# Kernel tuning notes

Hardware: AMD Instinct MI355X
Metric: run time of the kernel (lower is better)

The kernel has to match this reference:

```python
import jax, jax.numpy as jnp
import numpy as np

B = 65536
IN_DIM = 1280
E = 8          # num_experts
H1 = 256       # hidden_dim
H2 = 128       # hidden_dim // 2


def setup_inputs() -> dict:
    key = jax.random.key(0)
    ks = jax.random.split(key, 9)
    s1 = 1.0 / np.sqrt(IN_DIM)
    s2 = 1.0 / np.sqrt(H1)
    s3 = 1.0 / np.sqrt(H2)
    return {
        "x":  jax.random.normal(ks[0], (B, IN_DIM), dtype=jnp.float32),
        # stacked expert params: layer1 [E,in,H1], layer2 [E,H1,H2], layer3 [E,H2]
        "W1": jax.random.uniform(ks[1], (E, IN_DIM, H1), jnp.float32, -s1, s1),
        "b1": jax.random.uniform(ks[2], (E, H1), jnp.float32, -s1, s1),
        "W2": jax.random.uniform(ks[3], (E, H1, H2), jnp.float32, -s2, s2),
        "b2": jax.random.uniform(ks[4], (E, H2), jnp.float32, -s2, s2),
        "W3": jax.random.uniform(ks[5], (E, H2), jnp.float32, -s3, s3),
        "b3": jax.random.uniform(ks[6], (E,), jnp.float32, -s3, s3),
        # gate params [in,E]
        "Wg": jax.random.uniform(ks[7], (IN_DIM, E), jnp.float32, -s1, s1),
        "bg": jax.random.uniform(ks[8], (E,), jnp.float32, -s1, s1),
    }


def reference(x, W1, b1, W2, b2, W3, b3, Wg, bg):
    # All E experts run densely on every token (dropout = eval/identity).
    h1 = jax.nn.relu(jnp.einsum("bi,eih->beh", x, W1) + b1)          # [B,E,H1]
    h2 = jax.nn.relu(jnp.einsum("beh,ehk->bek", h1, W2) + b2)        # [B,E,H2]
    expert_out = jnp.einsum("bek,ek->be", h2, W3) + b3               # [B,E]
    gate = jax.nn.softmax(x @ Wg + bg, axis=-1)                      # [B,E]
    predictions = jnp.sum(expert_out * gate, axis=1)                 # [B]
    return predictions, gate
```

## Files before the change

kernel.cpp:

```cpp
#include <hip/hip_runtime.h>
#include <stdint.h>

#define NTOK 65536
#define KDIM 1280

typedef __attribute__((ext_vector_type(8))) short short8;
typedef __attribute__((ext_vector_type(4))) float floatx4;

__device__ __forceinline__ unsigned short f2bf(float f) {
  union { float f; unsigned int u; } v; v.f = f;
  unsigned int r = v.u + 0x7FFFu + ((v.u >> 16) & 1u);
  return (unsigned short)(r >> 16);
}

__device__ __forceinline__ unsigned cvtpk(float lo, float hi) {
  unsigned r;
  asm("v_cvt_pk_bf16_f32 %0, %1, %2" : "=v"(r) : "v"(lo), "v"(hi));
  return r;
}

#define GLDS16(gp, lp) \
  __builtin_amdgcn_global_load_lds((const __attribute__((address_space(1))) void*)(gp), \
                                   (__attribute__((address_space(3))) void*)(lp), 16, 0, 0)


__global__ __launch_bounds__(256)
void pack_all_kernel(const float* __restrict__ W1, const float* __restrict__ W2,
                     const float* __restrict__ Wg,
                     unsigned short* __restrict__ W1t, unsigned short* __restrict__ W2t,
                     unsigned short* __restrict__ WgTb) {
  int t = blockIdx.x * 256 + threadIdx.x;
  if (t < 327680) {
    int n = t / 160, kg = t - n * 160;
    int e = n >> 8, h = n & 255;
    int k = kg * 8;
    const float* src = W1 + ((size_t)e * 1280 + k) * 256 + h;
    uint4 o;
    o.x = (unsigned)f2bf(src[0])       | ((unsigned)f2bf(src[256])     << 16);
    o.y = (unsigned)f2bf(src[2 * 256]) | ((unsigned)f2bf(src[3 * 256]) << 16);
    o.z = (unsigned)f2bf(src[4 * 256]) | ((unsigned)f2bf(src[5 * 256]) << 16);
    o.w = (unsigned)f2bf(src[6 * 256]) | ((unsigned)f2bf(src[7 * 256]) << 16);
    *(uint4*)(W1t + (size_t)n * 1280 + k) = o;
  } else if (t < 360448) {
    int t2 = t - 327680;
    int ng = t2 >> 5, kg = t2 & 31;
    int e = ng >> 7, n = ng & 127;
    int k = kg * 8;
    const float* src = W2 + (size_t)e * 32768 + (size_t)k * 128 + n;
    uint4 o;
    o.x = (unsigned)f2bf(src[0])       | ((unsigned)f2bf(src[128])     << 16);
    o.y = (unsigned)f2bf(src[2 * 128]) | ((unsigned)f2bf(src[3 * 128]) << 16);
    o.z = (unsigned)f2bf(src[4 * 128]) | ((unsigned)f2bf(src[5 * 128]) << 16);
    o.w = (unsigned)f2bf(src[6 * 128]) | ((unsigned)f2bf(src[7 * 128]) << 16);
    *(uint4*)(W2t + (size_t)ng * 256 + k) = o;
  } else {
    int t3 = t - 360448;
    int e = t3 / 1280, k = t3 - e * 1280;
    WgTb[t3] = (e < 8) ? f2bf(Wg[(size_t)k * 8 + e]) : (unsigned short)0;
  }
}


__global__ __launch_bounds__(256, 3)
void expert_fused_kernel(const float* __restrict__ xf,
                         const unsigned short* __restrict__ W1t,
                         const float* __restrict__ b1,
                         const unsigned short* __restrict__ W2t,
                         const float* __restrict__ b2,
                         const float* __restrict__ W3,
                         const float* __restrict__ b3,
                         const unsigned short* __restrict__ WgTb,
                         const float* __restrict__ bg,
                         float* __restrict__ outG,
                         float* __restrict__ eo) {
  __shared__ __align__(16) unsigned short smem[24576];
  unsigned short* WsA = smem;
  unsigned short* WsB = smem + 8192;
  unsigned short* XsA = smem + 16384;
  unsigned short* XsB = smem + 18432;
  unsigned short* h1L = smem;
  unsigned short* W2A = smem + 16384;
  unsigned short* W2B = smem + 20480;
  unsigned short* WgA = smem + 20480;
  unsigned short* WgB = smem + 21504;

  const int tid = threadIdx.x;
  const int wv = tid >> 6;
  const int lane = tid & 63;

  const int wg = blockIdx.x + (blockIdx.y << 3);
  const int c  = wg & 7;
  const int w  = wg >> 3;
  const int e  = w & 7;
  const int m0 = ((c << 7) + (w >> 3)) << 6;
  const bool gate_blk = (e == 0);

  const unsigned short* W1te = W1t + (size_t)e * 256 * 1280;
  const unsigned short* W2te = W2t + (size_t)e * 128 * 256;

  const int lr = lane >> 2;
  const int ksw = ((lane & 3) ^ ((lane >> 3) & 3)) * 8;
  const int fr = lane & 15;
  const int fkS = (((lane >> 4) ^ ((lane >> 1) & 3)) & 3) * 8;
  const int fkL = (lane >> 4) * 8;
  const int rq = (lane >> 4) * 4;

  const float* gxf = xf + (size_t)(m0 + wv * 16 + lr) * 1280 + ksw;
  const unsigned short* gw = W1te + (size_t)(wv * 64 + lr) * 1280 + ksw;
  const unsigned short* gwg = WgTb + (size_t)lr * 1280 + ksw;
  unsigned short* lwA = &WsA[(wv * 64) * 32];
  unsigned short* lwB = &WsB[(wv * 64) * 32];
  const bool gate_stager = gate_blk && (wv == 0);

  floatx4 acc1[4][4] = {};
  floatx4 accg = {0.f, 0.f, 0.f, 0.f};
  for (int k0 = 0; k0 < 1280; k0 += 64) {
    float4 xa0 = *(const float4*)(gxf + k0);
    float4 xa1 = *(const float4*)(gxf + k0 + 4);
    float4 xb0 = *(const float4*)(gxf + k0 + 32);
    float4 xb1 = *(const float4*)(gxf + k0 + 36);
#pragma unroll
    for (int r = 0; r < 4; r++) {
      GLDS16(gw + (size_t)(16 * r) * 1280 + k0, lwA + r * 16 * 32);
      GLDS16(gw + (size_t)(16 * r) * 1280 + k0 + 32, lwB + r * 16 * 32);
    }
    if (gate_stager) { GLDS16(gwg + k0, WgA); GLDS16(gwg + k0 + 32, WgB); }
    uint4 pa, pb;
    pa.x = cvtpk(xa0.x, xa0.y); pa.y = cvtpk(xa0.z, xa0.w);
    pa.z = cvtpk(xa1.x, xa1.y); pa.w = cvtpk(xa1.z, xa1.w);
    pb.x = cvtpk(xb0.x, xb0.y); pb.y = cvtpk(xb0.z, xb0.w);
    pb.z = cvtpk(xb1.x, xb1.y); pb.w = cvtpk(xb1.z, xb1.w);
    *(uint4*)&XsA[(wv * 16 + lr) * 32 + (lane & 3) * 8] = pa;
    *(uint4*)&XsB[(wv * 16 + lr) * 32 + (lane & 3) * 8] = pb;
    __syncthreads();
    {
      short8 bfv[4];
#pragma unroll
      for (int j = 0; j < 4; j++)
        bfv[j] = *(const short8*)&XsA[(j * 16 + fr) * 32 + fkS];
#pragma unroll
      for (int i = 0; i < 4; i++) {
        short8 af = *(const short8*)&WsA[(wv * 64 + i * 16 + fr) * 32 + fkS];
#pragma unroll
        for (int j = 0; j < 4; j++)
          acc1[i][j] = __builtin_amdgcn_mfma_f32_16x16x32_bf16(af, bfv[j], acc1[i][j], 0, 0, 0);
      }
      if (gate_blk) {
        short8 ag = *(const short8*)&WgA[fr * 32 + fkS];
        short8 bgf = *(const short8*)&XsA[(wv * 16 + fr) * 32 + fkS];
        accg = __builtin_amdgcn_mfma_f32_16x16x32_bf16(ag, bgf, accg, 0, 0, 0);
      }
    }
    {
      short8 bfv[4];
#pragma unroll
      for (int j = 0; j < 4; j++)
        bfv[j] = *(const short8*)&XsB[(j * 16 + fr) * 32 + fkS];
#pragma unroll
      for (int i = 0; i < 4; i++) {
        short8 af = *(const short8*)&WsB[(wv * 64 + i * 16 + fr) * 32 + fkS];
#pragma unroll
        for (int j = 0; j < 4; j++)
          acc1[i][j] = __builtin_amdgcn_mfma_f32_16x16x32_bf16(af, bfv[j], acc1[i][j], 0, 0, 0);
      }
      if (gate_blk) {
        short8 ag = *(const short8*)&WgB[fr * 32 + fkS];
        short8 bgf = *(const short8*)&XsB[(wv * 16 + fr) * 32 + fkS];
        accg = __builtin_amdgcn_mfma_f32_16x16x32_bf16(ag, bgf, accg, 0, 0, 0);
      }
    }
    __syncthreads();
  }

  if (gate_blk) {
    const int g = lane >> 4;
    float bg0 = 0.f, bg1 = 0.f, bg2 = 0.f, bg3 = 0.f;
    if (g < 2) {
      float4 t = *(const float4*)(bg + g * 4);
      bg0 = t.x; bg1 = t.y; bg2 = t.z; bg3 = t.w;
    }
    float v0 = accg[0] + bg0, v1 = accg[1] + bg1, v2 = accg[2] + bg2, v3 = accg[3] + bg3;
    float mx = fmaxf(fmaxf(v0, v1), fmaxf(v2, v3));
    mx = fmaxf(mx, __shfl_xor(mx, 16));
    float e0 = __expf(v0 - mx), e1 = __expf(v1 - mx), e2 = __expf(v2 - mx), e3 = __expf(v3 - mx);
    float s = e0 + e1 + e2 + e3;
    s += __shfl_xor(s, 16);
    float inv = 1.f / s;
    if (g < 2) {
      float4 o; o.x = e0 * inv; o.y = e1 * inv; o.z = e2 * inv; o.w = e3 * inv;
      *(float4*)&outG[(size_t)(m0 + wv * 16 + fr) * 8 + g * 4] = o;
    }
  }

#pragma unroll
  for (int i = 0; i < 4; i++) {
    const int rowb = wv * 64 + i * 16 + rq;
    const float4 bb = *(const float4*)(b1 + e * 256 + rowb);
#pragma unroll
    for (int j = 0; j < 4; j++) {
      float v0 = acc1[i][j][0] + bb.x; v0 = v0 > 0.f ? v0 : 0.f;
      float v1 = acc1[i][j][1] + bb.y; v1 = v1 > 0.f ? v1 : 0.f;
      float v2 = acc1[i][j][2] + bb.z; v2 = v2 > 0.f ? v2 : 0.f;
      float v3 = acc1[i][j][3] + bb.w; v3 = v3 > 0.f ? v3 : 0.f;
      uint2 pk;
      pk.x = (unsigned)f2bf(v0) | ((unsigned)f2bf(v1) << 16);
      pk.y = (unsigned)f2bf(v2) | ((unsigned)f2bf(v3) << 16);
      const int row = j * 16 + fr;
      *(uint2*)((char*)h1L + ((row * 512 + rowb * 2) ^ ((row & 7) << 4))) = pk;
    }
  }
  __syncthreads();

  floatx4 acc2[2][4] = {};
  const unsigned short* gw2 = W2te + (size_t)(wv * 32 + lr) * 256 + ksw;
  unsigned short* lw2A = &W2A[(wv * 32) * 32];
  unsigned short* lw2B = &W2B[(wv * 32) * 32];
  for (int k0 = 0; k0 < 256; k0 += 64) {
    GLDS16(gw2 + k0, lw2A);
    GLDS16(gw2 + 16 * 256 + k0, lw2A + 16 * 32);
    GLDS16(gw2 + k0 + 32, lw2B);
    GLDS16(gw2 + 16 * 256 + k0 + 32, lw2B + 16 * 32);
    __syncthreads();
#pragma unroll
    for (int h = 0; h < 2; h++) {
      const unsigned short* W2s = h ? W2B : W2A;
      const int kk = k0 + h * 32;
      short8 b2v[4];
#pragma unroll
      for (int j = 0; j < 4; j++) {
        const int row = j * 16 + fr;
        b2v[j] = *(const short8*)((const char*)h1L +
                 ((row * 512 + (kk + fkL) * 2) ^ ((row & 7) << 4)));
      }
#pragma unroll
      for (int i = 0; i < 2; i++) {
        short8 a2 = *(const short8*)&W2s[(wv * 32 + i * 16 + fr) * 32 + fkS];
#pragma unroll
        for (int j = 0; j < 4; j++)
          acc2[i][j] = __builtin_amdgcn_mfma_f32_16x16x32_bf16(a2, b2v[j], acc2[i][j], 0, 0, 0);
      }
    }
    __syncthreads();
  }

  float psum[4] = {0.f, 0.f, 0.f, 0.f};
#pragma unroll
  for (int i = 0; i < 2; i++) {
    const int rowb = wv * 32 + i * 16 + rq;
    const float4 bb = *(const float4*)(b2 + e * 128 + rowb);
    const float4 ww = *(const float4*)(W3 + e * 128 + rowb);
    const float bba[4] = {bb.x, bb.y, bb.z, bb.w};
    const float wwa[4] = {ww.x, ww.y, ww.z, ww.w};
#pragma unroll
    for (int j = 0; j < 4; j++)
#pragma unroll
      for (int r = 0; r < 4; r++) {
        float v = acc2[i][j][r] + bba[r];
        v = v > 0.f ? v : 0.f;
        psum[j] += v * wwa[r];
      }
  }
#pragma unroll
  for (int j = 0; j < 4; j++) {
    float v = psum[j];
    v += __shfl_xor(v, 16);
    v += __shfl_xor(v, 32);
    psum[j] = v;
  }
  float* exS = (float*)XsA;
  if (lane < 16) {
#pragma unroll
    for (int j = 0; j < 4; j++) exS[wv * 64 + j * 16 + lane] = psum[j];
  }
  __syncthreads();
  if (tid < 64) {
    float tot = exS[tid] + exS[64 + tid] + exS[128 + tid] + exS[192 + tid];
    eo[(size_t)(m0 + tid) * 8 + e] = tot + b3[e];
  }
}


__global__ __launch_bounds__(256)
void combine_kernel(const float* __restrict__ outG, const float* __restrict__ eo,
                    float* __restrict__ outP) {
  int t = blockIdx.x * 256 + threadIdx.x;
  const float4* g4 = (const float4*)(outG + (size_t)t * 8);
  const float4* e4 = (const float4*)(eo + (size_t)t * 8);
  float4 ga = g4[0], gb = g4[1], ea = e4[0], eb = e4[1];
  outP[t] = ga.x * ea.x + ga.y * ea.y + ga.z * ea.z + ga.w * ea.w +
            gb.x * eb.x + gb.y * eb.y + gb.z * eb.z + gb.w * eb.w;
}


extern "C" void kernel_launch(void* const* d_in, const int* in_sizes, int n_in,
                              void* d_out, int out_size, void* d_ws, size_t ws_size,
                              hipStream_t stream) {
  const float* x  = (const float*)d_in[0];
  const float* W1 = (const float*)d_in[1];
  const float* b1 = (const float*)d_in[2];
  const float* W2 = (const float*)d_in[3];
  const float* b2 = (const float*)d_in[4];
  const float* W3 = (const float*)d_in[5];
  const float* b3 = (const float*)d_in[6];
  const float* Wg = (const float*)d_in[7];
  const float* bg = (const float*)d_in[8];
  float* outP = (float*)d_out;
  float* outG = outP + NTOK;

  char* ws = (char*)d_ws;
  unsigned short* W1t  = (unsigned short*)ws;
  unsigned short* W2t  = (unsigned short*)(ws + 5242880ll);
  unsigned short* WgTb = (unsigned short*)(ws + 5767168ll);
  float*          eo   = (float*)(ws + 5808128ll);

  pack_all_kernel<<<1488, 256, 0, stream>>>(W1, W2, Wg, W1t, W2t, WgTb);
  expert_fused_kernel<<<dim3(8, 1024), 256, 0, stream>>>(x, W1t, b1, W2t, b2, W3, b3,
                                                         WgTb, bg, outG, eo);
  combine_kernel<<<256, 256, 0, stream>>>(outG, eo, outP);
}
```

Measured before the change: 890.4 us.

## Load expert weights directly into registers and double-buffer X tile in LDS

```diff
diff --git a/kernel.cpp b/kernel.cpp
--- a/kernel.cpp
+++ b/kernel.cpp
@@ -18,10 +18,6 @@
   asm("v_cvt_pk_bf16_f32 %0, %1, %2" : "=v"(r) : "v"(lo), "v"(hi));
   return r;
 }
-
-#define GLDS16(gp, lp) \
-  __builtin_amdgcn_global_load_lds((const __attribute__((address_space(1))) void*)(gp), \
-                                   (__attribute__((address_space(3))) void*)(lp), 16, 0, 0)
 
 
 __global__ __launch_bounds__(256)
@@ -74,15 +70,8 @@
                          float* __restrict__ outG,
                          float* __restrict__ eo) {
   __shared__ __align__(16) unsigned short smem[24576];
-  unsigned short* WsA = smem;
-  unsigned short* WsB = smem + 8192;
-  unsigned short* XsA = smem + 16384;
-  unsigned short* XsB = smem + 18432;
-  unsigned short* h1L = smem;
-  unsigned short* W2A = smem + 16384;
-  unsigned short* W2B = smem + 20480;
-  unsigned short* WgA = smem + 20480;
-  unsigned short* WgB = smem + 21504;
+  unsigned short* Xs  = smem;
+  unsigned short* h1L = smem + 8192;
 
   const int tid = threadIdx.x;
   const int wv = tid >> 6;
@@ -91,8 +80,10 @@
   const int wg = blockIdx.x + (blockIdx.y << 3);
   const int c  = wg & 7;
   const int w  = wg >> 3;
-  const int e  = w & 7;
-  const int m0 = ((c << 7) + (w >> 3)) << 6;
+  const int chunk = w >> 7;
+  const int w7 = w & 127;
+  const int e  = w7 >> 4;
+  const int m0 = ((c << 7) + (chunk << 4) + (w7 & 15)) << 6;
   const bool gate_blk = (e == 0);
 
   const unsigned short* W1te = W1t + (size_t)e * 256 * 1280;
@@ -106,68 +97,68 @@
   const int rq = (lane >> 4) * 4;
 
   const float* gxf = xf + (size_t)(m0 + wv * 16 + lr) * 1280 + ksw;
-  const unsigned short* gw = W1te + (size_t)(wv * 64 + lr) * 1280 + ksw;
-  const unsigned short* gwg = WgTb + (size_t)lr * 1280 + ksw;
-  unsigned short* lwA = &WsA[(wv * 64) * 32];
-  unsigned short* lwB = &WsB[(wv * 64) * 32];
-  const bool gate_stager = gate_blk && (wv == 0);
+  const int xslot = (wv * 16 + lr) * 32 + (lane & 3) * 8;
+  const unsigned short* gw1 = W1te + (size_t)(wv * 64 + fr) * 1280 + fkL;
+  const unsigned short* gwg = WgTb + (size_t)fr * 1280 + fkL;
 
   floatx4 acc1[4][4] = {};
   floatx4 accg = {0.f, 0.f, 0.f, 0.f};
-  for (int k0 = 0; k0 < 1280; k0 += 64) {
-    float4 xa0 = *(const float4*)(gxf + k0);
-    float4 xa1 = *(const float4*)(gxf + k0 + 4);
-    float4 xb0 = *(const float4*)(gxf + k0 + 32);
-    float4 xb1 = *(const float4*)(gxf + k0 + 36);
-#pragma unroll
-    for (int r = 0; r < 4; r++) {
-      GLDS16(gw + (size_t)(16 * r) * 1280 + k0, lwA + r * 16 * 32);
-      GLDS16(gw + (size_t)(16 * r) * 1280 + k0 + 32, lwB + r * 16 * 32);
-    }
-    if (gate_stager) { GLDS16(gwg + k0, WgA); GLDS16(gwg + k0 + 32, WgB); }
+
+  {
+    float4 a0 = *(const float4*)(gxf);
+    float4 a1 = *(const float4*)(gxf + 4);
+    float4 b0 = *(const float4*)(gxf + 32);
+    float4 b1v = *(const float4*)(gxf + 36);
     uint4 pa, pb;
-    pa.x = cvtpk(xa0.x, xa0.y); pa.y = cvtpk(xa0.z, xa0.w);
-    pa.z = cvtpk(xa1.x, xa1.y); pa.w = cvtpk(xa1.z, xa1.w);
-    pb.x = cvtpk(xb0.x, xb0.y); pb.y = cvtpk(xb0.z, xb0.w);
-    pb.z = cvtpk(xb1.x, xb1.y); pb.w = cvtpk(xb1.z, xb1.w);
-    *(uint4*)&XsA[(wv * 16 + lr) * 32 + (lane & 3) * 8] = pa;
-    *(uint4*)&XsB[(wv * 16 + lr) * 32 + (lane & 3) * 8] = pb;
-    __syncthreads();
-    {
+    pa.x = cvtpk(a0.x, a0.y); pa.y = cvtpk(a0.z, a0.w);
+    pa.z = cvtpk(a1.x, a1.y); pa.w = cvtpk(a1.z, a1.w);
+    pb.x = cvtpk(b0.x, b0.y); pb.y = cvtpk(b0.z, b0.w);
+    pb.z = cvtpk(b1v.x, b1v.y); pb.w = cvtpk(b1v.z, b1v.w);
+    *(uint4*)&Xs[xslot] = pa;
+    *(uint4*)&Xs[2048 + xslot] = pb;
+  }
+  __syncthreads();
+
+  for (int t = 0; t < 20; ++t) {
+    const int k0 = t * 64;
+    const int cur = (t & 1) << 12;
+    float4 na0, na1, nb0, nb1;
+    if (t < 19) {
+      na0 = *(const float4*)(gxf + k0 + 64);
+      na1 = *(const float4*)(gxf + k0 + 68);
+      nb0 = *(const float4*)(gxf + k0 + 96);
+      nb1 = *(const float4*)(gxf + k0 + 100);
+    }
+#pragma unroll
+    for (int s = 0; s < 2; ++s) {
+      const int kk = k0 + s * 32;
+      const int xbase = cur + (s << 11);
       short8 bfv[4];
 #pragma unroll
       for (int j = 0; j < 4; j++)
-        bfv[j] = *(const short8*)&XsA[(j * 16 + fr) * 32 + fkS];
+        bfv[j] = *(const short8*)&Xs[xbase + (j * 16 + fr) * 32 + fkS];
 #pragma unroll
       for (int i = 0; i < 4; i++) {
-        short8 af = *(const short8*)&WsA[(wv * 64 + i * 16 + fr) * 32 + fkS];
+        short8 af = *(const short8*)(gw1 + (size_t)(i * 16) * 1280 + kk);
 #pragma unroll
         for (int j = 0; j < 4; j++)
           acc1[i][j] = __builtin_amdgcn_mfma_f32_16x16x32_bf16(af, bfv[j], acc1[i][j], 0, 0, 0);
       }
       if (gate_blk) {
-        short8 ag = *(const short8*)&WgA[fr * 32 + fkS];
-        short8 bgf = *(const short8*)&XsA[(wv * 16 + fr) * 32 + fkS];
+        short8 ag = *(const short8*)(gwg + kk);
+        short8 bgf = *(const short8*)&Xs[xbase + (wv * 16 + fr) * 32 + fkS];
         accg = __builtin_amdgcn_mfma_f32_16x16x32_bf16(ag, bgf, accg, 0, 0, 0);
       }
     }
-    {
-      short8 bfv[4];
-#pragma unroll
-      for (int j = 0; j < 4; j++)
-        bfv[j] = *(const short8*)&XsB[(j * 16 + fr) * 32 + fkS];
-#pragma unroll
-      for (int i = 0; i < 4; i++) {
-        short8 af = *(const short8*)&WsB[(wv * 64 + i * 16 + fr) * 32 + fkS];
-#pragma unroll
-        for (int j = 0; j < 4; j++)
-          acc1[i][j] = __builtin_amdgcn_mfma_f32_16x16x32_bf16(af, bfv[j], acc1[i][j], 0, 0, 0);
-      }
-      if (gate_blk) {
-        short8 ag = *(const short8*)&WgB[fr * 32 + fkS];
-        short8 bgf = *(const short8*)&XsB[(wv * 16 + fr) * 32 + fkS];
-        accg = __builtin_amdgcn_mfma_f32_16x16x32_bf16(ag, bgf, accg, 0, 0, 0);
-      }
+    if (t < 19) {
+      const int nxt = cur ^ 4096;
+      uint4 pa, pb;
+      pa.x = cvtpk(na0.x, na0.y); pa.y = cvtpk(na0.z, na0.w);
+      pa.z = cvtpk(na1.x, na1.y); pa.w = cvtpk(na1.z, na1.w);
+      pb.x = cvtpk(nb0.x, nb0.y); pb.y = cvtpk(nb0.z, nb0.w);
+      pb.z = cvtpk(nb1.x, nb1.y); pb.w = cvtpk(nb1.z, nb1.w);
+      *(uint4*)&Xs[nxt + xslot] = pa;
+      *(uint4*)&Xs[nxt + 2048 + xslot] = pb;
     }
     __syncthreads();
   }
@@ -212,35 +203,23 @@
   __syncthreads();
 
   floatx4 acc2[2][4] = {};
-  const unsigned short* gw2 = W2te + (size_t)(wv * 32 + lr) * 256 + ksw;
-  unsigned short* lw2A = &W2A[(wv * 32) * 32];
-  unsigned short* lw2B = &W2B[(wv * 32) * 32];
-  for (int k0 = 0; k0 < 256; k0 += 64) {
-    GLDS16(gw2 + k0, lw2A);
-    GLDS16(gw2 + 16 * 256 + k0, lw2A + 16 * 32);
-    GLDS16(gw2 + k0 + 32, lw2B);
-    GLDS16(gw2 + 16 * 256 + k0 + 32, lw2B + 16 * 32);
-    __syncthreads();
-#pragma unroll
-    for (int h = 0; h < 2; h++) {
-      const unsigned short* W2s = h ? W2B : W2A;
-      const int kk = k0 + h * 32;
-      short8 b2v[4];
-#pragma unroll
-      for (int j = 0; j < 4; j++) {
-        const int row = j * 16 + fr;
-        b2v[j] = *(const short8*)((const char*)h1L +
-                 ((row * 512 + (kk + fkL) * 2) ^ ((row & 7) << 4)));
-      }
-#pragma unroll
-      for (int i = 0; i < 2; i++) {
-        short8 a2 = *(const short8*)&W2s[(wv * 32 + i * 16 + fr) * 32 + fkS];
-#pragma unroll
-        for (int j = 0; j < 4; j++)
-          acc2[i][j] = __builtin_amdgcn_mfma_f32_16x16x32_bf16(a2, b2v[j], acc2[i][j], 0, 0, 0);
-      }
-    }
-    __syncthreads();
+  const unsigned short* gw2 = W2te + (size_t)(wv * 32 + fr) * 256 + fkL;
+#pragma unroll
+  for (int k0 = 0; k0 < 256; k0 += 32) {
+    short8 b2v[4];
+#pragma unroll
+    for (int j = 0; j < 4; j++) {
+      const int row = j * 16 + fr;
+      b2v[j] = *(const short8*)((const char*)h1L +
+               ((row * 512 + (k0 + fkL) * 2) ^ ((row & 7) << 4)));
+    }
+#pragma unroll
+    for (int i = 0; i < 2; i++) {
+      short8 a2 = *(const short8*)(gw2 + (size_t)(i * 16) * 256 + k0);
+#pragma unroll
+      for (int j = 0; j < 4; j++)
+        acc2[i][j] = __builtin_amdgcn_mfma_f32_16x16x32_bf16(a2, b2v[j], acc2[i][j], 0, 0, 0);
+    }
   }
 
   float psum[4] = {0.f, 0.f, 0.f, 0.f};
@@ -267,7 +246,7 @@
     v += __shfl_xor(v, 32);
     psum[j] = v;
   }
-  float* exS = (float*)XsA;
+  float* exS = (float*)Xs;
   if (lane < 16) {
 #pragma unroll
     for (int j = 0; j < 4; j++) exS[wv * 64 + j * 16 + lane] = psum[j];
```

Result: slower. 1.167 ms (+31.0%).
